# Performance work log

Hardware: AMD Instinct MI355X
Metric: run time of the kernel (lower is better)

The kernel has to match this reference:

```python
import jax, jax.numpy as jnp
import numpy as np

H = 16
DH = 64


def setup_inputs() -> dict:
    key = jax.random.key(0)
    ks = jax.random.split(key, 8)
    b, n, m, d = 2, 2048, 2048, 1024
    inner = H * DH  # 1024
    return {
        "x": jax.random.normal(ks[0], (b, n, d), jnp.float32),
        "mem_k": jax.random.normal(ks[1], (b, m, inner), jnp.float32),
        "mem_v": jax.random.normal(ks[2], (b, m, inner), jnp.float32),
        "Wq": jax.random.normal(ks[3], (d, inner), jnp.float32) * (d ** -0.5),
        "Wkv": jax.random.normal(ks[4], (d, 2 * inner), jnp.float32) * (d ** -0.5),
        "b_kv": jax.random.normal(ks[5], (2 * inner,), jnp.float32) * 0.02,
        "Wo": jax.random.normal(ks[6], (inner, d), jnp.float32) * (inner ** -0.5),
        "b_o": jax.random.normal(ks[7], (d,), jnp.float32) * 0.02,
    }


def reference(x, mem_k, mem_v, Wq, Wkv, b_kv, Wo, b_o):
    b, n, d = x.shape
    scale = DH ** -0.5
    q = (x @ Wq) * scale                       # [b, n, h*dh]
    self_k, self_v = jnp.split(x @ Wkv + b_kv, 2, axis=-1)
    k = jnp.concatenate([mem_k, self_k], axis=1)   # [b, j, h*dh]
    v = jnp.concatenate([mem_v, self_v], axis=1)

    def split_heads(t):
        return t.reshape(b, t.shape[1], H, DH).transpose(0, 2, 1, 3)  # b h n d

    q, k, v = map(split_heads, (q, k, v))
    sim = jnp.einsum('bhid,bhjd->bhij', q, k)  # [b, h, n, j]
    i, j = sim.shape[-2:]
    # causal mask: query i may attend to keys up to position (j - i) + i
    causal_mask = jnp.triu(jnp.ones((i, j), dtype=bool), k=j - i + 1)
    mask_value = -jnp.finfo(sim.dtype).max
    sim = jnp.where(causal_mask[None, None], mask_value, sim)
    attn = jax.nn.softmax(sim, axis=-1)
    out = jnp.einsum('bhij,bhjd->bhid', attn, v)
    out = out.transpose(0, 2, 1, 3).reshape(b, n, H * DH)
    return out @ Wo + b_o
```

## Files before the change

### kernel.cpp

```cpp
#include <hip/hip_runtime.h>
#include <stdint.h>

typedef __bf16 bf16x8 __attribute__((ext_vector_type(8)));
typedef _Float16 f16x8 __attribute__((ext_vector_type(8)));
typedef float f32x4 __attribute__((ext_vector_type(4)));
typedef float f32x16 __attribute__((ext_vector_type(16)));

constexpr int Mm = 2048;
constexpr float QSCALE = 0.18033688011112042f;

__device__ __forceinline__ float exp2_fast(float x) {
  return __builtin_amdgcn_exp2f(x);
}

__device__ __forceinline__ uint16_t f2bf(float f) {
  union { float f; uint32_t u; } v; v.f = f;
  return (uint16_t)((v.u + 0x7FFFu + ((v.u >> 16) & 1u)) >> 16);
}
__device__ __forceinline__ uint32_t pack2(float a, float b) {
  return (uint32_t)f2bf(a) | ((uint32_t)f2bf(b) << 16);
}
__device__ __forceinline__ uint32_t pkrtz(float a, float b) {
  auto h2 = __builtin_amdgcn_cvt_pkrtz(a, b);
  return __builtin_bit_cast(uint32_t, h2);
}
__device__ __forceinline__ uint16_t f2h(float f) {
  _Float16 h = (_Float16)f;
  return __builtin_bit_cast(uint16_t, h);
}

__device__ __forceinline__ void async16(const void* g, void* l) {
  __builtin_amdgcn_global_load_lds(
      (__attribute__((address_space(1))) uint32_t*)g,
      (__attribute__((address_space(3))) uint32_t*)l, 16, 0, 0);
}

__device__ __forceinline__ bf16x8 frag64(const uint16_t* base, int row, int chunk) {
  return *(const bf16x8*)(base + row * 64 + chunk * 8);
}
__device__ __forceinline__ f16x8 frag64h(const uint16_t* base, int row, int chunk) {
  return *(const f16x8*)(base + row * 64 + chunk * 8);
}

__global__ __launch_bounds__(256) void prep_kernel(
    const float* __restrict__ x, const float* __restrict__ mem_k,
    const float* __restrict__ mem_v, const float* __restrict__ Wq,
    const float* __restrict__ Wkv, const float* __restrict__ Wo,
    uint16_t* __restrict__ Xb, uint16_t* __restrict__ WallT,
    uint16_t* __restrict__ WoT, uint16_t* __restrict__ Kh,
    uint16_t* __restrict__ VhT) {
  __shared__ float tile[64][65];
  __shared__ uint16_t vtile[64 * 66];
  const int tid = threadIdx.x;
  int blk = blockIdx.x;

  if (blk < 1024) {
    const float4* x4 = (const float4*)x;
    for (int it = 0; it < 4; ++it) {
      int idx4 = blk * 1024 + it * 256 + tid;
      float4 v = x4[idx4];
      uint2 w; w.x = pack2(v.x, v.y); w.y = pack2(v.z, v.w);
      ((uint2*)Xb)[idx4] = w;
    }
    return;
  }
  blk -= 1024;
  if (blk < 1024) {
    const float* src; uint16_t* dst; int ld, colbase, n0, k0;
    if (blk < 768) {
      int nt = blk >> 4, kt = blk & 15;
      n0 = nt * 64; k0 = kt * 64;
      if (n0 < 1024) { src = Wq; ld = 1024; colbase = n0; }
      else           { src = Wkv; ld = 2048; colbase = n0 - 1024; }
      dst = WallT;
    } else {
      int b2 = blk - 768;
      int nt = b2 >> 4, kt = b2 & 15;
      n0 = nt * 64; k0 = kt * 64;
      src = Wo; ld = 1024; colbase = n0; dst = WoT;
    }
    int r = tid >> 4, c = (tid & 15) * 4;
    for (int it = 0; it < 4; ++it) {
      int rr = r + it * 16;
      float4 v = *(const float4*)(src + (size_t)(k0 + rr) * ld + colbase + c);
      tile[rr][c] = v.x; tile[rr][c + 1] = v.y;
      tile[rr][c + 2] = v.z; tile[rr][c + 3] = v.w;
    }
    __syncthreads();
    for (int it = 0; it < 4; ++it) {
      int rn = r + it * 16;
      uint2 w;
      w.x = pack2(tile[c][rn], tile[c + 1][rn]);
      w.y = pack2(tile[c + 2][rn], tile[c + 3][rn]);
      *(uint2*)(dst + (size_t)(n0 + rn) * 1024 + k0 + c) = w;
    }
    return;
  }
  blk -= 1024;
  if (blk < 1024) {
    const float4* s4 = (const float4*)mem_k;
    for (int it = 0; it < 4; ++it) {
      int idx4 = blk * 1024 + it * 256 + tid;
      int e = idx4 * 4;
      int b = e >> 21;
      int rem = e & ((1 << 21) - 1);
      int m = rem >> 10;
      int cc = rem & 1023;
      int h = cc >> 6, dh = cc & 63;
      float4 v = s4[idx4];
      uint2 w; w.x = pack2(v.x, v.y); w.y = pack2(v.z, v.w);
      *(uint2*)(Kh + (((size_t)(b * 16 + h) * 4096) + m) * 64 + dh) = w;
    }
    return;
  }
  blk -= 1024;
  {
    const int b = blk >> 9, h = (blk >> 5) & 15, m0 = (blk & 31) * 64;
    const float4* s4 = (const float4*)mem_v;
    for (int it = 0; it < 4; ++it) {
      int idx = it * 256 + tid;
      int r = idx >> 4, d4 = (idx & 15) * 4;
      float4 v = s4[(size_t)(b * 2048 + m0 + r) * 256 + h * 16 + (d4 >> 2)];
      *(uint32_t*)&vtile[r * 66 + d4]     = pkrtz(v.x, v.y);
      *(uint32_t*)&vtile[r * 66 + d4 + 2] = pkrtz(v.z, v.w);
    }
    __syncthreads();
    int d = tid & 63;
    for (int half = 0; half < 2; ++half) {
      int mg = (tid >> 6) + half * 4;
      uint32_t w[4];
      for (int p = 0; p < 4; ++p) {
        uint32_t lo = vtile[(mg * 8 + 2 * p) * 66 + d];
        uint32_t hi = vtile[(mg * 8 + 2 * p + 1) * 66 + d];
        w[p] = lo | (hi << 16);
      }
      *(uint4*)&VhT[((size_t)((b * 16 + h) * 64) + d) * 4096 + m0 + mg * 8] =
          *(uint4*)w;
    }
  }
}

template <int MODE>
__global__ __launch_bounds__(256) void gemm_kernel(
    const uint16_t* __restrict__ A, const uint16_t* __restrict__ Bt,
    const float* __restrict__ bias, uint16_t* __restrict__ Qh,
    uint16_t* __restrict__ Kh, uint16_t* __restrict__ VhT,
    float* __restrict__ Out) {
  constexpr int K = 1024;
  constexpr int SS = 136;
  constexpr int BM = (MODE == 0) ? 128 : 64;
  constexpr int MT = BM / 32;
  constexpr int CPT = (BM + 128) * 8 / 256;
  const int m0 = blockIdx.x * BM, n0 = blockIdx.y * 128;
  const int tid = threadIdx.x;
  const int wave = tid >> 6, lane = tid & 63;
  const int lhi = lane >> 4, llo = lane & 15;
  const int wm = (wave >> 1) * (BM / 2), wn = (wave & 1) * 64;

  __shared__ uint16_t sh[MODE == 0 ? 128 * SS : (64 + 128) * 64];
  uint16_t* As = sh;
  uint16_t* Bs = sh + BM * 64;

  f32x4 acc[MT][4] = {};

  for (int kt = 0; kt < K / 64; ++kt) {
    __syncthreads();
    for (int c = 0; c < CPT; ++c) {
      int cl = c * 256 + tid;
      if (cl < BM * 8) {
        int row = cl >> 3, ch = cl & 7;
        async16(A + (size_t)(m0 + row) * K + kt * 64 + ch * 8, As + cl * 8);
      } else {
        int bl = cl - BM * 8;
        int row = bl >> 3, ch = bl & 7;
        async16(Bt + (size_t)(n0 + row) * K + kt * 64 + ch * 8, Bs + bl * 8);
      }
    }
    __syncthreads();
    for (int ks = 0; ks < 2; ++ks) {
      bf16x8 af[MT], bfr[4];
      for (int mt = 0; mt < MT; ++mt) af[mt] = frag64(As, wm + mt * 16 + llo, ks * 4 + lhi);
      for (int nt = 0; nt < 4; ++nt) bfr[nt] = frag64(Bs, wn + nt * 16 + llo, ks * 4 + lhi);
      for (int mt = 0; mt < MT; ++mt)
        for (int nt = 0; nt < 4; ++nt)
          acc[mt][nt] = __builtin_amdgcn_mfma_f32_16x16x32_bf16(af[mt], bfr[nt], acc[mt][nt], 0, 0, 0);
    }
  }

  if (MODE == 0) {
    const int region = n0 >> 10;
    __syncthreads();
    for (int nt = 0; nt < 4; ++nt) {
      int cloc = wn + nt * 16 + llo;
      int col = n0 + cloc;
      float badd = (region == 0) ? 0.f : bias[col - 1024];
      for (int mt = 0; mt < 4; ++mt) {
        int rloc = wm + mt * 16 + lhi * 4;
        for (int reg = 0; reg < 4; ++reg) {
          float v = acc[mt][nt][reg];
          v = (region == 0) ? v * QSCALE : v + badd;
          if (region == 2) sh[cloc * SS + rloc + reg] = f2h(v);
          else             sh[(rloc + reg) * SS + cloc] = f2bf(v);
        }
      }
    }
    __syncthreads();
    if (region == 2) {
      const int rl = (tid & 15) * 8;
      for (int it = 0; it < 8; ++it) {
        int cloc = (tid >> 4) + it * 16;
        int col = n0 + cloc;
        int cc = col - 2048, h = cc >> 6, dh = cc & 63;
        int r = m0 + rl;
        int b = r >> 11, n = r & 2047;
        uint4 w = *(const uint4*)&sh[cloc * SS + rl];
        *(uint4*)&VhT[((size_t)((b * 16 + h) * 64) + dh) * 4096 + 2048 + n] = w;
      }
    } else {
      const int cl16 = (tid & 15) * 8;
      const int col = n0 + cl16;
      for (int it = 0; it < 8; ++it) {
        int rloc = (tid >> 4) + it * 16;
        int r = m0 + rloc;
        int b = r >> 11, n = r & 2047;
        uint4 w = *(const uint4*)&sh[rloc * SS + cl16];
        if (region == 0) {
          int h = col >> 6, dh = col & 63;
          *(uint4*)&Qh[(((size_t)(b * 16 + h) * 2048) + n) * 64 + dh] = w;
        } else {
          int cc = col - 1024, h = cc >> 6, dh = cc & 63;
          *(uint4*)&Kh[(((size_t)(b * 16 + h) * 4096) + 2048 + n) * 64 + dh] = w;
        }
      }
    }
  } else {
    for (int nt = 0; nt < 4; ++nt) {
      int col = n0 + wn + nt * 16 + llo;
      float bo = bias[col];
      for (int mt = 0; mt < MT; ++mt) {
        int rbase = m0 + wm + mt * 16 + lhi * 4;
        for (int reg = 0; reg < 4; ++reg)
          Out[(size_t)(rbase + reg) * 1024 + col] = acc[mt][nt][reg] + bo;
      }
    }
  }
}

__global__ __launch_bounds__(256, 2) void attn_kernel(
    const uint16_t* __restrict__ Qh, const uint16_t* __restrict__ Kh,
    const uint16_t* __restrict__ VhT, uint16_t* __restrict__ AO) {
  const int bh = blockIdx.x;
  const int qt = (blockIdx.y < 8) ? (15 - (int)blockIdx.y)
                                  : ((int)blockIdx.y - 8);
  const int tid = threadIdx.x;
  const int wave = tid >> 6, lane = tid & 63;
  const int lo5 = lane & 31, hi = lane >> 5;
  const int qg = wave & 1, kp = wave >> 1;
  const int i0 = qt * 128;
  const int swz5 = lo5 & 7;

  __shared__ uint16_t Ks[2][2][64 * 64];
  __shared__ uint16_t Vt[2][2][64 * 64];

  bf16x8 qf0[4], qf1[4];
  {
    const uint16_t* Qw0 = Qh + ((size_t)bh * 2048 + i0 + qg * 64 + lo5) * 64;
    const uint16_t* Qw1 = Qw0 + 32 * 64;
#pragma unroll
    for (int k = 0; k < 4; ++k) {
      qf0[k] = *(const bf16x8*)(Qw0 + k * 16 + hi * 8);
      qf1[k] = *(const bf16x8*)(Qw1 + k * 16 + hi * 8);
    }
  }

  const uint16_t* Kbh = Kh + (size_t)bh * 4096 * 64;
  const uint16_t* Vbh = VhT + (size_t)bh * 64 * 4096;

  f32x16 o00 = {}, o01 = {}, o10 = {}, o11 = {};
  float l0p = 0.f, l1p = 0.f;

  const int npairs = 17 + qt;

  auto stage = [&](int buf, int u_) {
    const int arr = wave >> 1;
    const int par = wave & 1;
    const int kk0 = u_ * 128 + par * 64;
    uint16_t* dstb = arr == 0 ? &Ks[buf][par][0] : &Vt[buf][par][0];
#pragma unroll
    for (int c = 0; c < 8; ++c) {
      int row = c * 8 + (lane >> 3);
      int chs = (lane & 7) ^ (row & 7);
      const uint16_t* src = arr == 0
          ? Kbh + (size_t)(kk0 + row) * 64 + chs * 8
          : Vbh + (size_t)row * 4096 + kk0 + chs * 8;
      async16(src, dstb + c * 512);
    }
  };

  stage(0, 0);

  const int iw0 = i0 + qg * 64;
  const int iw1 = iw0 + 32;

  for (int u = 0; u < npairs; ++u) {
    const int cur = u & 1;
    __syncthreads();
    if (u + 1 < npairs) stage(cur ^ 1, u + 1);

    const int k0t = (2 * u + kp) * 64;
    const uint16_t* Kt = &Ks[cur][kp][0];
    const uint16_t* Vtt = &Vt[cur][kp][0];

    uint32_t pw0[2][2][4], pw1[2][2][4];

#pragma unroll
    for (int mblk = 0; mblk < 2; ++mblk) {
      f32x16 s0v = {}, s1v = {};
      __builtin_amdgcn_s_setprio(1);
#pragma unroll
      for (int kstep = 0; kstep < 4; ++kstep) {
        bf16x8 kf = frag64(Kt, mblk * 32 + lo5, (2 * kstep + hi) ^ swz5);
        s0v = __builtin_amdgcn_mfma_f32_32x32x16_bf16(kf, qf0[kstep], s0v, 0, 0, 0);
        s1v = __builtin_amdgcn_mfma_f32_32x32x16_bf16(kf, qf1[kstep], s1v, 0, 0, 0);
      }
      __builtin_amdgcn_s_setprio(0);

      if (k0t + mblk * 32 + 31 > Mm + iw0) {
        const int lim = Mm + iw0 + lo5 - k0t - mblk * 32;
#pragma unroll
        for (int r = 0; r < 16; ++r) {
          int kl = (r & 3) + 8 * (r >> 2) + 4 * hi;
          if (kl > lim) s0v[r] = -INFINITY;
        }
      }
      if (k0t + mblk * 32 + 31 > Mm + iw1) {
        const int lim = Mm + iw1 + lo5 - k0t - mblk * 32;
#pragma unroll
        for (int r = 0; r < 16; ++r) {
          int kl = (r & 3) + 8 * (r >> 2) + 4 * hi;
          if (kl > lim) s1v[r] = -INFINITY;
        }
      }

      float e0[16], e1[16];
#pragma unroll
      for (int r = 0; r < 16; ++r) { e0[r] = exp2_fast(s0v[r]); e1[r] = exp2_fast(s1v[r]); }
      {
        float a0 = (e0[0] + e0[1]) + (e0[2] + e0[3]);
        float a1 = (e0[4] + e0[5]) + (e0[6] + e0[7]);
        float a2 = (e0[8] + e0[9]) + (e0[10] + e0[11]);
        float a3 = (e0[12] + e0[13]) + (e0[14] + e0[15]);
        l0p += (a0 + a1) + (a2 + a3);
        float b0 = (e1[0] + e1[1]) + (e1[2] + e1[3]);
        float b1 = (e1[4] + e1[5]) + (e1[6] + e1[7]);
        float b2 = (e1[8] + e1[9]) + (e1[10] + e1[11]);
        float b3 = (e1[12] + e1[13]) + (e1[14] + e1[15]);
        l1p += (b0 + b1) + (b2 + b3);
      }

      uint32_t c0[8], c1[8];
#pragma unroll
      for (int w = 0; w < 8; ++w) {
        c0[w] = pkrtz(e0[2 * w], e0[2 * w + 1]);
        c1[w] = pkrtz(e1[2 * w], e1[2 * w + 1]);
      }
#pragma unroll
      for (int kk2 = 0; kk2 < 2; ++kk2) {
        uint32_t a0 = c0[4 * kk2 + 0], a2 = c0[4 * kk2 + 2];
        uint32_t a1 = c0[4 * kk2 + 1], a3 = c0[4 * kk2 + 3];
        asm volatile("v_permlane32_swap_b32 %0, %1" : "+v"(a0), "+v"(a2));
        asm volatile("v_permlane32_swap_b32 %0, %1" : "+v"(a1), "+v"(a3));
        pw0[mblk][kk2][0] = a0; pw0[mblk][kk2][1] = a1;
        pw0[mblk][kk2][2] = a2; pw0[mblk][kk2][3] = a3;
        uint32_t b0 = c1[4 * kk2 + 0], b2 = c1[4 * kk2 + 2];
        uint32_t b1 = c1[4 * kk2 + 1], b3 = c1[4 * kk2 + 3];
        asm volatile("v_permlane32_swap_b32 %0, %1" : "+v"(b0), "+v"(b2));
        asm volatile("v_permlane32_swap_b32 %0, %1" : "+v"(b1), "+v"(b3));
        pw1[mblk][kk2][0] = b0; pw1[mblk][kk2][1] = b1;
        pw1[mblk][kk2][2] = b2; pw1[mblk][kk2][3] = b3;
      }
    }

#pragma unroll
    for (int mblk = 0; mblk < 2; ++mblk)
#pragma unroll
      for (int kk2 = 0; kk2 < 2; ++kk2) {
        const int kk = mblk * 2 + kk2;
        uint4 fwa; fwa.x = pw0[mblk][kk2][0]; fwa.y = pw0[mblk][kk2][1];
        fwa.z = pw0[mblk][kk2][2]; fwa.w = pw0[mblk][kk2][3];
        f16x8 pa0 = __builtin_bit_cast(f16x8, fwa);
        uint4 fwb; fwb.x = pw1[mblk][kk2][0]; fwb.y = pw1[mblk][kk2][1];
        fwb.z = pw1[mblk][kk2][2]; fwb.w = pw1[mblk][kk2][3];
        f16x8 pa1 = __builtin_bit_cast(f16x8, fwb);
        f16x8 vf0 = frag64h(Vtt, lo5,      (2 * kk + hi) ^ swz5);
        f16x8 vf1 = frag64h(Vtt, 32 + lo5, (2 * kk + hi) ^ swz5);
        __builtin_amdgcn_s_setprio(1);
        o00 = __builtin_amdgcn_mfma_f32_32x32x16_f16(pa0, vf0, o00, 0, 0, 0);
        o01 = __builtin_amdgcn_mfma_f32_32x32x16_f16(pa0, vf1, o01, 0, 0, 0);
        o10 = __builtin_amdgcn_mfma_f32_32x32x16_f16(pa1, vf0, o10, 0, 0, 0);
        o11 = __builtin_amdgcn_mfma_f32_32x32x16_f16(pa1, vf1, o11, 0, 0, 0);
        __builtin_amdgcn_s_setprio(0);
      }
  }

  float l0full, l1full;
  {
    float a0 = l0p, b0 = l0p;
    asm volatile("v_permlane32_swap_b32 %0, %1" : "+v"(a0), "+v"(b0));
    l0full = a0 + b0;
    float a1 = l1p, b1 = l1p;
    asm volatile("v_permlane32_swap_b32 %0, %1" : "+v"(a1), "+v"(b1));
    l1full = a1 + b1;
  }

  const int b = bh >> 4, h = bh & 15;
  float* F = (float*)&Ks[0][0][0];
  float* L = (float*)&Vt[1][0][0];
  uint16_t* Es = &Vt[0][0][0];

  __syncthreads();
  if (hi == 0) {
    L[kp * 128 + qg * 64 + lo5]      = l0full;
    L[kp * 128 + qg * 64 + 32 + lo5] = l1full;
  }
  if (kp == 1) {
#pragma unroll
    for (int r = 0; r < 16; ++r) {
      int q0 = qg * 64 + (r & 3) + 8 * (r >> 2) + 4 * hi;
      int q1 = q0 + 32;
      F[q0 * 64 + lo5]      = o00[r];
      F[q0 * 64 + 32 + lo5] = o01[r];
      F[q1 * 64 + lo5]      = o10[r];
      F[q1 * 64 + 32 + lo5] = o11[r];
    }
  }
  __syncthreads();
  if (kp == 0) {
#pragma unroll
    for (int r = 0; r < 16; ++r) {
      int q0 = qg * 64 + (r & 3) + 8 * (r >> 2) + 4 * hi;
      int q1 = q0 + 32;
      float inv0 = 1.0f / (L[q0] + L[128 + q0]);
      float inv1 = 1.0f / (L[q1] + L[128 + q1]);
      Es[q0 * 64 + lo5]      = f2bf((o00[r] + F[q0 * 64 + lo5]) * inv0);
      Es[q0 * 64 + 32 + lo5] = f2bf((o01[r] + F[q0 * 64 + 32 + lo5]) * inv0);
      Es[q1 * 64 + lo5]      = f2bf((o10[r] + F[q1 * 64 + lo5]) * inv1);
      Es[q1 * 64 + 32 + lo5] = f2bf((o11[r] + F[q1 * 64 + 32 + lo5]) * inv1);
    }
  }
  __syncthreads();
  {
    int row = tid >> 1, c32 = (tid & 1) * 32;
    size_t base = ((size_t)(b * 2048) + i0 + row) * 1024 + h * 64 + c32;
    *(uint4*)&AO[base]      = *(const uint4*)&Es[row * 64 + c32];
    *(uint4*)&AO[base + 8]  = *(const uint4*)&Es[row * 64 + c32 + 8];
    *(uint4*)&AO[base + 16] = *(const uint4*)&Es[row * 64 + c32 + 16];
    *(uint4*)&AO[base + 24] = *(const uint4*)&Es[row * 64 + c32 + 24];
  }
}

extern "C" void kernel_launch(void* const* d_in, const int* in_sizes, int n_in,
                              void* d_out, int out_size, void* d_ws,
                              size_t ws_size, hipStream_t stream) {
  const float* x     = (const float*)d_in[0];
  const float* mem_k = (const float*)d_in[1];
  const float* mem_v = (const float*)d_in[2];
  const float* Wq    = (const float*)d_in[3];
  const float* Wkv   = (const float*)d_in[4];
  const float* b_kv  = (const float*)d_in[5];
  const float* Wo    = (const float*)d_in[6];
  const float* b_o   = (const float*)d_in[7];
  float* out = (float*)d_out;

  char* ws = (char*)d_ws;
  uint16_t* Xb    = (uint16_t*)(ws);
  uint16_t* WallT = (uint16_t*)(ws + (8ull << 20));
  uint16_t* WoT   = (uint16_t*)(ws + (14ull << 20));
  uint16_t* Qh    = (uint16_t*)(ws + (16ull << 20));
  uint16_t* Kh    = (uint16_t*)(ws + (24ull << 20));
  uint16_t* VhT   = (uint16_t*)(ws + (40ull << 20));
  uint16_t* AO    = (uint16_t*)(ws + (56ull << 20));

  prep_kernel<<<4096, 256, 0, stream>>>(x, mem_k, mem_v, Wq, Wkv, Wo,
                                        Xb, WallT, WoT, Kh, VhT);
  gemm_kernel<0><<<dim3(32, 24), 256, 0, stream>>>(Xb, WallT, b_kv,
                                                   Qh, Kh, VhT, nullptr);
  attn_kernel<<<dim3(32, 16), 256, 0, stream>>>(Qh, Kh, VhT, AO);
  gemm_kernel<1><<<dim3(64, 8), 256, 0, stream>>>(AO, WoT, b_o,
                                                  nullptr, nullptr, nullptr, out);
}
```

Baseline: 240.9 us.

## Split attention key blocks across 8 waves with a tree reduction of partial outputs

```diff
diff --git a/kernel.cpp b/kernel.cpp
--- a/kernel.cpp
+++ b/kernel.cpp
@@ -246,7 +246,7 @@
   }
 }
 
-__global__ __launch_bounds__(256, 2) void attn_kernel(
+__global__ __launch_bounds__(512, 4) void attn_kernel(
     const uint16_t* __restrict__ Qh, const uint16_t* __restrict__ Kh,
     const uint16_t* __restrict__ VhT, uint16_t* __restrict__ AO) {
   const int bh = blockIdx.x;
@@ -255,12 +255,14 @@
   const int tid = threadIdx.x;
   const int wave = tid >> 6, lane = tid & 63;
   const int lo5 = lane & 31, hi = lane >> 5;
-  const int qg = wave & 1, kp = wave >> 1;
+  const int qg = wave & 1, kp = (wave >> 1) & 1, mblk = wave >> 2;
   const int i0 = qt * 128;
   const int swz5 = lo5 & 7;
 
-  __shared__ uint16_t Ks[2][2][64 * 64];
-  __shared__ uint16_t Vt[2][2][64 * 64];
+  __shared__ __align__(16) unsigned char smem[67584];
+  uint16_t* KsB = (uint16_t*)smem;
+  uint16_t* VtB = (uint16_t*)(smem + 32768);
+  float* Ls = (float*)(smem + 65536);
 
   bf16x8 qf0[4], qf1[4];
   {
@@ -282,18 +284,20 @@
   const int npairs = 17 + qt;
 
   auto stage = [&](int buf, int u_) {
-    const int arr = wave >> 1;
-    const int par = wave & 1;
+    const int arr = wave >> 2;
+    const int par = (wave >> 1) & 1;
+    const int half = wave & 1;
     const int kk0 = u_ * 128 + par * 64;
-    uint16_t* dstb = arr == 0 ? &Ks[buf][par][0] : &Vt[buf][par][0];
-#pragma unroll
-    for (int c = 0; c < 8; ++c) {
-      int row = c * 8 + (lane >> 3);
-      int chs = (lane & 7) ^ (row & 7);
+    uint16_t* dstb = (arr == 0 ? KsB : VtB) + (buf * 2 + par) * 4096;
+#pragma unroll
+    for (int c = 0; c < 4; ++c) {
+      int lc = half * 256 + c * 64 + lane;
+      int row = lc >> 3, ch = lc & 7;
+      int chs = ch ^ (row & 7);
       const uint16_t* src = arr == 0
           ? Kbh + (size_t)(kk0 + row) * 64 + chs * 8
           : Vbh + (size_t)row * 4096 + kk0 + chs * 8;
-      async16(src, dstb + c * 512);
+      async16(src, dstb + lc * 8);
     }
   };
 
@@ -308,99 +312,83 @@
     if (u + 1 < npairs) stage(cur ^ 1, u + 1);
 
     const int k0t = (2 * u + kp) * 64;
-    const uint16_t* Kt = &Ks[cur][kp][0];
-    const uint16_t* Vtt = &Vt[cur][kp][0];
-
-    uint32_t pw0[2][2][4], pw1[2][2][4];
-
-#pragma unroll
-    for (int mblk = 0; mblk < 2; ++mblk) {
-      f32x16 s0v = {}, s1v = {};
+    const uint16_t* Kt = KsB + (cur * 2 + kp) * 4096;
+    const uint16_t* Vtt = VtB + (cur * 2 + kp) * 4096;
+
+    f32x16 s0v = {}, s1v = {};
+    __builtin_amdgcn_s_setprio(1);
+#pragma unroll
+    for (int kstep = 0; kstep < 4; ++kstep) {
+      bf16x8 kf = frag64(Kt, mblk * 32 + lo5, (2 * kstep + hi) ^ swz5);
+      s0v = __builtin_amdgcn_mfma_f32_32x32x16_bf16(kf, qf0[kstep], s0v, 0, 0, 0);
+      s1v = __builtin_amdgcn_mfma_f32_32x32x16_bf16(kf, qf1[kstep], s1v, 0, 0, 0);
+    }
+    __builtin_amdgcn_s_setprio(0);
+
+    if (k0t + mblk * 32 + 31 > Mm + iw0) {
+      const int lim = Mm + iw0 + lo5 - k0t - mblk * 32;
+#pragma unroll
+      for (int r = 0; r < 16; ++r) {
+        int kl = (r & 3) + 8 * (r >> 2) + 4 * hi;
+        if (kl > lim) s0v[r] = -INFINITY;
+      }
+    }
+    if (k0t + mblk * 32 + 31 > Mm + iw1) {
+      const int lim = Mm + iw1 + lo5 - k0t - mblk * 32;
+#pragma unroll
+      for (int r = 0; r < 16; ++r) {
+        int kl = (r & 3) + 8 * (r >> 2) + 4 * hi;
+        if (kl > lim) s1v[r] = -INFINITY;
+      }
+    }
+
+    float e0[16], e1[16];
+#pragma unroll
+    for (int r = 0; r < 16; ++r) { e0[r] = exp2_fast(s0v[r]); e1[r] = exp2_fast(s1v[r]); }
+    {
+      float a0 = (e0[0] + e0[1]) + (e0[2] + e0[3]);
+      float a1 = (e0[4] + e0[5]) + (e0[6] + e0[7]);
+      float a2 = (e0[8] + e0[9]) + (e0[10] + e0[11]);
+      float a3 = (e0[12] + e0[13]) + (e0[14] + e0[15]);
+      l0p += (a0 + a1) + (a2 + a3);
+      float b0 = (e1[0] + e1[1]) + (e1[2] + e1[3]);
+      float b1 = (e1[4] + e1[5]) + (e1[6] + e1[7]);
+      float b2 = (e1[8] + e1[9]) + (e1[10] + e1[11]);
+      float b3 = (e1[12] + e1[13]) + (e1[14] + e1[15]);
+      l1p += (b0 + b1) + (b2 + b3);
+    }
+
+    uint32_t c0[8], c1[8];
+#pragma unroll
+    for (int w = 0; w < 8; ++w) {
+      c0[w] = pkrtz(e0[2 * w], e0[2 * w + 1]);
+      c1[w] = pkrtz(e1[2 * w], e1[2 * w + 1]);
+    }
+#pragma unroll
+    for (int kk2 = 0; kk2 < 2; ++kk2) {
+      uint32_t a0 = c0[4 * kk2 + 0], a2 = c0[4 * kk2 + 2];
+      uint32_t a1 = c0[4 * kk2 + 1], a3 = c0[4 * kk2 + 3];
+      asm volatile("v_permlane32_swap_b32 %0, %1" : "+v"(a0), "+v"(a2));
+      asm volatile("v_permlane32_swap_b32 %0, %1" : "+v"(a1), "+v"(a3));
+      uint4 fwa; fwa.x = a0; fwa.y = a1; fwa.z = a2; fwa.w = a3;
+      f16x8 pa0 = __builtin_bit_cast(f16x8, fwa);
+      uint32_t b0 = c1[4 * kk2 + 0], b2 = c1[4 * kk2 + 2];
+      uint32_t b1 = c1[4 * kk2 + 1], b3 = c1[4 * kk2 + 3];
+      asm volatile("v_permlane32_swap_b32 %0, %1" : "+v"(b0), "+v"(b2));
+      asm volatile("v_permlane32_swap_b32 %0, %1" : "+v"(b1), "+v"(b3));
+      uint4 fwb; fwb.x = b0; fwb.y = b1; fwb.z = b2; fwb.w = b3;
+      f16x8 pa1 = __builtin_bit_cast(f16x8, fwb);
+
+      const int kk = mblk * 2 + kk2;
+      f16x8 vf0 = frag64h(Vtt, lo5,      (2 * kk + hi) ^ swz5);
+      f16x8 vf1 = frag64h(Vtt, 32 + lo5, (2 * kk + hi) ^ swz5);
       __builtin_amdgcn_s_setprio(1);
-#pragma unroll
-      for (int kstep = 0; kstep < 4; ++kstep) {
-        bf16x8 kf = frag64(Kt, mblk * 32 + lo5, (2 * kstep + hi) ^ swz5);
-        s0v = __builtin_amdgcn_mfma_f32_32x32x16_bf16(kf, qf0[kstep], s0v, 0, 0, 0);
-        s1v = __builtin_amdgcn_mfma_f32_32x32x16_bf16(kf, qf1[kstep], s1v, 0, 0, 0);
-      }
+      o00 = __builtin_amdgcn_mfma_f32_32x32x16_f16(pa0, vf0, o00, 0, 0, 0);
+      o01 = __builtin_amdgcn_mfma_f32_32x32x16_f16(pa0, vf1, o01, 0, 0, 0);
+      o10 = __builtin_amdgcn_mfma_f32_32x32x16_f16(pa1, vf0, o10, 0, 0, 0);
+      o11 = __builtin_amdgcn_mfma_f32_32x32x16_f16(pa1, vf1, o11, 0, 0, 0);
       __builtin_amdgcn_s_setprio(0);
-
-      if (k0t + mblk * 32 + 31 > Mm + iw0) {
-        const int lim = Mm + iw0 + lo5 - k0t - mblk * 32;
-#pragma unroll
-        for (int r = 0; r < 16; ++r) {
-          int kl = (r & 3) + 8 * (r >> 2) + 4 * hi;
-          if (kl > lim) s0v[r] = -INFINITY;
-        }
-      }
-      if (k0t + mblk * 32 + 31 > Mm + iw1) {
-        const int lim = Mm + iw1 + lo5 - k0t - mblk * 32;
-#pragma unroll
-        for (int r = 0; r < 16; ++r) {
-          int kl = (r & 3) + 8 * (r >> 2) + 4 * hi;
-          if (kl > lim) s1v[r] = -INFINITY;
-        }
-      }
-
-      float e0[16], e1[16];
-#pragma unroll
-      for (int r = 0; r < 16; ++r) { e0[r] = exp2_fast(s0v[r]); e1[r] = exp2_fast(s1v[r]); }
-      {
-        float a0 = (e0[0] + e0[1]) + (e0[2] + e0[3]);
-        float a1 = (e0[4] + e0[5]) + (e0[6] + e0[7]);
-        float a2 = (e0[8] + e0[9]) + (e0[10] + e0[11]);
-        float a3 = (e0[12] + e0[13]) + (e0[14] + e0[15]);
-        l0p += (a0 + a1) + (a2 + a3);
-        float b0 = (e1[0] + e1[1]) + (e1[2] + e1[3]);
-        float b1 = (e1[4] + e1[5]) + (e1[6] + e1[7]);
-        float b2 = (e1[8] + e1[9]) + (e1[10] + e1[11]);
-        float b3 = (e1[12] + e1[13]) + (e1[14] + e1[15]);
-        l1p += (b0 + b1) + (b2 + b3);
-      }
-
-      uint32_t c0[8], c1[8];
-#pragma unroll
-      for (int w = 0; w < 8; ++w) {
-        c0[w] = pkrtz(e0[2 * w], e0[2 * w + 1]);
-        c1[w] = pkrtz(e1[2 * w], e1[2 * w + 1]);
-      }
-#pragma unroll
-      for (int kk2 = 0; kk2 < 2; ++kk2) {
-        uint32_t a0 = c0[4 * kk2 + 0], a2 = c0[4 * kk2 + 2];
-        uint32_t a1 = c0[4 * kk2 + 1], a3 = c0[4 * kk2 + 3];
-        asm volatile("v_permlane32_swap_b32 %0, %1" : "+v"(a0), "+v"(a2));
-        asm volatile("v_permlane32_swap_b32 %0, %1" : "+v"(a1), "+v"(a3));
-        pw0[mblk][kk2][0] = a0; pw0[mblk][kk2][1] = a1;
-        pw0[mblk][kk2][2] = a2; pw0[mblk][kk2][3] = a3;
-        uint32_t b0 = c1[4 * kk2 + 0], b2 = c1[4 * kk2 + 2];
-        uint32_t b1 = c1[4 * kk2 + 1], b3 = c1[4 * kk2 + 3];
-        asm volatile("v_permlane32_swap_b32 %0, %1" : "+v"(b0), "+v"(b2));
-        asm volatile("v_permlane32_swap_b32 %0, %1" : "+v"(b1), "+v"(b3));
-        pw1[mblk][kk2][0] = b0; pw1[mblk][kk2][1] = b1;
-        pw1[mblk][kk2][2] = b2; pw1[mblk][kk2][3] = b3;
-      }
-    }
-
-#pragma unroll
-    for (int mblk = 0; mblk < 2; ++mblk)
-#pragma unroll
-      for (int kk2 = 0; kk2 < 2; ++kk2) {
-        const int kk = mblk * 2 + kk2;
-        uint4 fwa; fwa.x = pw0[mblk][kk2][0]; fwa.y = pw0[mblk][kk2][1];
-        fwa.z = pw0[mblk][kk2][2]; fwa.w = pw0[mblk][kk2][3];
-        f16x8 pa0 = __builtin_bit_cast(f16x8, fwa);
-        uint4 fwb; fwb.x = pw1[mblk][kk2][0]; fwb.y = pw1[mblk][kk2][1];
-        fwb.z = pw1[mblk][kk2][2]; fwb.w = pw1[mblk][kk2][3];
-        f16x8 pa1 = __builtin_bit_cast(f16x8, fwb);
-        f16x8 vf0 = frag64h(Vtt, lo5,      (2 * kk + hi) ^ swz5);
-        f16x8 vf1 = frag64h(Vtt, 32 + lo5, (2 * kk + hi) ^ swz5);
-        __builtin_amdgcn_s_setprio(1);
-        o00 = __builtin_amdgcn_mfma_f32_32x32x16_f16(pa0, vf0, o00, 0, 0, 0);
-        o01 = __builtin_amdgcn_mfma_f32_32x32x16_f16(pa0, vf1, o01, 0, 0, 0);
-        o10 = __builtin_amdgcn_mfma_f32_32x32x16_f16(pa1, vf0, o10, 0, 0, 0);
-        o11 = __builtin_amdgcn_mfma_f32_32x32x16_f16(pa1, vf1, o11, 0, 0, 0);
-        __builtin_amdgcn_s_setprio(0);
-      }
+    }
   }
 
   float l0full, l1full;
@@ -414,48 +402,80 @@
   }
 
   const int b = bh >> 4, h = bh & 15;
-  float* F = (float*)&Ks[0][0][0];
-  float* L = (float*)&Vt[1][0][0];
-  uint16_t* Es = &Vt[0][0][0];
+  float* F = (float*)smem;
+  uint16_t* Es = (uint16_t*)smem;
 
   __syncthreads();
   if (hi == 0) {
-    L[kp * 128 + qg * 64 + lo5]      = l0full;
-    L[kp * 128 + qg * 64 + 32 + lo5] = l1full;
-  }
-  if (kp == 1) {
+    Ls[((qg * 2 + kp) * 2 + mblk) * 64 + lo5]      = l0full;
+    Ls[((qg * 2 + kp) * 2 + mblk) * 64 + 32 + lo5] = l1full;
+  }
+  if (mblk == 1) {
+    float* Fr = F + (qg * 2 + kp) * 4096;
 #pragma unroll
     for (int r = 0; r < 16; ++r) {
-      int q0 = qg * 64 + (r & 3) + 8 * (r >> 2) + 4 * hi;
+      int q0 = (r & 3) + 8 * (r >> 2) + 4 * hi;
       int q1 = q0 + 32;
-      F[q0 * 64 + lo5]      = o00[r];
-      F[q0 * 64 + 32 + lo5] = o01[r];
-      F[q1 * 64 + lo5]      = o10[r];
-      F[q1 * 64 + 32 + lo5] = o11[r];
+      Fr[q0 * 64 + lo5]      = o00[r];
+      Fr[q0 * 64 + 32 + lo5] = o01[r];
+      Fr[q1 * 64 + lo5]      = o10[r];
+      Fr[q1 * 64 + 32 + lo5] = o11[r];
     }
   }
   __syncthreads();
-  if (kp == 0) {
+  if (mblk == 0) {
+    float* Fr = F + (qg * 2 + kp) * 4096;
 #pragma unroll
     for (int r = 0; r < 16; ++r) {
-      int q0 = qg * 64 + (r & 3) + 8 * (r >> 2) + 4 * hi;
+      int q0 = (r & 3) + 8 * (r >> 2) + 4 * hi;
       int q1 = q0 + 32;
-      float inv0 = 1.0f / (L[q0] + L[128 + q0]);
-      float inv1 = 1.0f / (L[q1] + L[128 + q1]);
-      Es[q0 * 64 + lo5]      = f2bf((o00[r] + F[q0 * 64 + lo5]) * inv0);
-      Es[q0 * 64 + 32 + lo5] = f2bf((o01[r] + F[q0 * 64 + 32 + lo5]) * inv0);
-      Es[q1 * 64 + lo5]      = f2bf((o10[r] + F[q1 * 64 + lo5]) * inv1);
-      Es[q1 * 64 + 32 + lo5] = f2bf((o11[r] + F[q1 * 64 + 32 + lo5]) * inv1);
+      o00[r] += Fr[q0 * 64 + lo5];
+      o01[r] += Fr[q0 * 64 + 32 + lo5];
+      o10[r] += Fr[q1 * 64 + lo5];
+      o11[r] += Fr[q1 * 64 + 32 + lo5];
+    }
+    if (kp == 1) {
+#pragma unroll
+      for (int r = 0; r < 16; ++r) {
+        int q0 = (r & 3) + 8 * (r >> 2) + 4 * hi;
+        int q1 = q0 + 32;
+        Fr[q0 * 64 + lo5]      = o00[r];
+        Fr[q0 * 64 + 32 + lo5] = o01[r];
+        Fr[q1 * 64 + lo5]      = o10[r];
+        Fr[q1 * 64 + 32 + lo5] = o11[r];
+      }
+    }
+  }
+  __syncthreads();
+  if (mblk == 0 && kp == 0) {
+    float* Fo = F + (qg * 2 + 1) * 4096;
+#pragma unroll
+    for (int r = 0; r < 16; ++r) {
+      int q0 = (r & 3) + 8 * (r >> 2) + 4 * hi;
+      int q1 = q0 + 32;
+      float lt0 = Ls[((qg * 2 + 0) * 2 + 0) * 64 + q0] +
+                  Ls[((qg * 2 + 0) * 2 + 1) * 64 + q0] +
+                  Ls[((qg * 2 + 1) * 2 + 0) * 64 + q0] +
+                  Ls[((qg * 2 + 1) * 2 + 1) * 64 + q0];
+      float lt1 = Ls[((qg * 2 + 0) * 2 + 0) * 64 + q1] +
+                  Ls[((qg * 2 + 0) * 2 + 1) * 64 + q1] +
+                  Ls[((qg * 2 + 1) * 2 + 0) * 64 + q1] +
+                  Ls[((qg * 2 + 1) * 2 + 1) * 64 + q1];
+      float inv0 = 1.0f / lt0;
+      float inv1 = 1.0f / lt1;
+      int qq0 = qg * 64 + q0, qq1 = qg * 64 + q1;
+      Es[qq0 * 64 + lo5]      = f2bf((o00[r] + Fo[q0 * 64 + lo5]) * inv0);
+      Es[qq0 * 64 + 32 + lo5] = f2bf((o01[r] + Fo[q0 * 64 + 32 + lo5]) * inv0);
+      Es[qq1 * 64 + lo5]      = f2bf((o10[r] + Fo[q1 * 64 + lo5]) * inv1);
+      Es[qq1 * 64 + 32 + lo5] = f2bf((o11[r] + Fo[q1 * 64 + 32 + lo5]) * inv1);
     }
   }
   __syncthreads();
   {
-    int row = tid >> 1, c32 = (tid & 1) * 32;
-    size_t base = ((size_t)(b * 2048) + i0 + row) * 1024 + h * 64 + c32;
-    *(uint4*)&AO[base]      = *(const uint4*)&Es[row * 64 + c32];
-    *(uint4*)&AO[base + 8]  = *(const uint4*)&Es[row * 64 + c32 + 8];
-    *(uint4*)&AO[base + 16] = *(const uint4*)&Es[row * 64 + c32 + 16];
-    *(uint4*)&AO[base + 24] = *(const uint4*)&Es[row * 64 + c32 + 24];
+    int row = tid >> 2, seg = (tid & 3) * 16;
+    size_t base = ((size_t)(b * 2048) + i0 + row) * 1024 + h * 64 + seg;
+    *(uint4*)&AO[base]     = *(const uint4*)&Es[row * 64 + seg];
+    *(uint4*)&AO[base + 8] = *(const uint4*)&Es[row * 64 + seg + 8];
   }
 }
 
@@ -485,7 +505,7 @@
                                         Xb, WallT, WoT, Kh, VhT);
   gemm_kernel<0><<<dim3(32, 24), 256, 0, stream>>>(Xb, WallT, b_kv,
                                                    Qh, Kh, VhT, nullptr);
-  attn_kernel<<<dim3(32, 16), 256, 0, stream>>>(Qh, Kh, VhT, AO);
+  attn_kernel<<<dim3(32, 16), 512, 0, stream>>>(Qh, Kh, VhT, AO);
   gemm_kernel<1><<<dim3(64, 8), 256, 0, stream>>>(AO, WoT, b_o,
                                                   nullptr, nullptr, nullptr, out);
 }
```

Result: slower. 458.4 us (+90.3%).
